# Optimization experiments

Measured on AMD Instinct MI355X. Metric: run time of the kernel, lower is better.

The kernel has to match this reference:

```python
import jax, jax.numpy as jnp
import numpy as np
from jax import lax

LR, SB, LB = 256, 16, 8  # lr_size, spatial_bin, luma_bins
DN = ('NCHW', 'OIHW', 'NCHW')


def conv2d(x, w, b=None, stride=1, pad=1):
    out = lax.conv_general_dilated(x, w, (stride, stride), [(pad, pad), (pad, pad)], dimension_numbers=DN)
    return out if b is None else out + b[None, :, None, None]


def gaussian_blur17(x):
    # kornia GaussianBlur2d(kernel=(17,17), sigma=(2,2)), reflect padding, separable
    t = jnp.arange(17, dtype=x.dtype) - 8.0
    g = jnp.exp(-(t * t) / 8.0)  # 2*sigma^2 = 8
    g = g / g.sum()
    C = x.shape[1]
    xp = jnp.pad(x, ((0, 0), (0, 0), (8, 8), (8, 8)), mode='reflect')
    kh = jnp.broadcast_to(g.reshape(1, 1, 17, 1), (C, 1, 17, 1))
    kw = jnp.broadcast_to(g.reshape(1, 1, 1, 17), (C, 1, 1, 17))
    x1 = lax.conv_general_dilated(xp, kh, (1, 1), 'VALID', dimension_numbers=DN, feature_group_count=C)
    return lax.conv_general_dilated(x1, kw, (1, 1), 'VALID', dimension_numbers=DN, feature_group_count=C)


def nearest_resize(x, size):
    # torch F.interpolate mode='nearest': src = floor(dst * in/out)
    H, W = x.shape[-2], x.shape[-1]
    iy = jnp.floor(jnp.arange(size) * (H / size)).astype(jnp.int32)
    ix = jnp.floor(jnp.arange(size) * (W / size)).astype(jnp.int32)
    return x[:, :, iy][:, :, :, ix]


def grid_sample_3d_border(inp, grid):
    # inp [B,C,D,Hi,Wi]; grid [B,Do,Ho,Wo,3] with (x,y,z); bilinear, padding_mode='border', align_corners=False
    B, C, D, Hi, Wi = inp.shape
    x = jnp.clip(((grid[..., 0] + 1.0) * Wi - 1.0) * 0.5, 0.0, Wi - 1.0)
    y = jnp.clip(((grid[..., 1] + 1.0) * Hi - 1.0) * 0.5, 0.0, Hi - 1.0)
    z = jnp.clip(((grid[..., 2] + 1.0) * D - 1.0) * 0.5, 0.0, D - 1.0)
    x0 = jnp.floor(x); y0 = jnp.floor(y); z0 = jnp.floor(z)
    fx = (x - x0)[:, None]; fy = (y - y0)[:, None]; fz = (z - z0)[:, None]  # [B,1,Do,Ho,Wo]
    x0i = x0.astype(jnp.int32); y0i = y0.astype(jnp.int32); z0i = z0.astype(jnp.int32)
    x1i = jnp.minimum(x0i + 1, Wi - 1); y1i = jnp.minimum(y0i + 1, Hi - 1); z1i = jnp.minimum(z0i + 1, D - 1)
    flat = inp.reshape(B, C, D * Hi * Wi)
    M = grid.shape[1] * grid.shape[2] * grid.shape[3]

    def gat(zi, yi, xi):
        idx = ((zi * Hi + yi) * Wi + xi).reshape(B, 1, M)
        v = jnp.take_along_axis(flat, jnp.broadcast_to(idx, (B, C, M)), axis=2)
        return v.reshape(B, C, grid.shape[1], grid.shape[2], grid.shape[3])

    return (gat(z0i, y0i, x0i) * (1 - fz) * (1 - fy) * (1 - fx)
            + gat(z0i, y0i, x1i) * (1 - fz) * (1 - fy) * fx
            + gat(z0i, y1i, x0i) * (1 - fz) * fy * (1 - fx)
            + gat(z0i, y1i, x1i) * (1 - fz) * fy * fx
            + gat(z1i, y0i, x0i) * fz * (1 - fy) * (1 - fx)
            + gat(z1i, y0i, x1i) * fz * (1 - fy) * fx
            + gat(z1i, y1i, x0i) * fz * fy * (1 - fx)
            + gat(z1i, y1i, x1i) * fz * fy * fx)


def _forward(lqs, evs, gw1, gb1, gw2, gb2, sw0, sb0, sw1, sb1, sw2, sb2, sw3, sb3,
             cw0, cb0, cw1, cb1, fw1, fb1, fw2, fb2, fw3, fb3, lw1, lb1, lw2, fuw, fub):
    B, _, H, W = lqs.shape
    # --- HighresStreamNet guide ---
    g = gaussian_blur17(lqs)
    g = jax.nn.relu(conv2d(g, gw1, gb1, 1, 0))
    guide = jax.nn.sigmoid(conv2d(g, gw2, gb2, 1, 0)) * 2.0 - 0.5  # [B,1,H,W]
    # --- slicing grid (x,y in (-0.5,1.5) per source, z = guide) ---
    gx = (jnp.arange(W, dtype=lqs.dtype) + 0.5) / W * 2.0 - 0.5
    gy = (jnp.arange(H, dtype=lqs.dtype) + 0.5) / H * 2.0 - 0.5
    gyy, gxx = jnp.meshgrid(gy, gx, indexing='ij')
    base = jnp.broadcast_to(jnp.stack([gxx, gyy], -1)[None, None], (B, 1, H, W, 2))
    grid = jnp.concatenate([base, guide[..., None]], axis=-1)  # [B,1,H,W,3]
    # --- LowresStreamNet ---
    lr = nearest_resize(lqs, LR)
    ev = evs if (evs.shape[-1] == LR and evs.shape[-2] == LR) else nearest_resize(evs, LR)
    x = jnp.concatenate([lr, ev], axis=1)  # [B,18,256,256]
    for w_, b_ in ((sw0, sb0), (sw1, sb1), (sw2, sb2), (sw3, sb3)):
        x = jax.nn.relu(conv2d(x, w_, b_, 2, 1))  # -> [B,64,16,16]
    xl = conv2d(jax.nn.relu(conv2d(x, lw1, lb1, 1, 1)), lw2, None, 1, 1)  # local, last conv no bias
    xg = jax.nn.relu(conv2d(x, cw0, cb0, 2, 1))
    xg = jax.nn.relu(conv2d(xg, cw1, cb1, 2, 1)).reshape(B, -1)  # [B,1024]
    xg = jax.nn.relu(xg @ fw1.T + fb1)
    xg = jax.nn.relu(xg @ fw2.T + fb2)
    xg = xg @ fw3.T + fb3  # [B,64]
    fused = jax.nn.relu(xg[:, :, None, None] + xl)
    bg = conv2d(fused, fuw, fub, 1, 0).reshape(B, 1, LB, SB, SB)  # bilateral grid [B,1,8,16,16]
    hr = grid_sample_3d_border(bg, grid)  # [B,1,1,H,W]
    return hr.reshape(B, -1, H, W)


def setup_inputs():
    key = jax.random.key(0)
    ks = iter(jax.random.split(key, 40))

    def W_(shape):
        fan_in = int(np.prod(shape[1:]))
        return jax.random.normal(next(ks), shape, jnp.float32) * np.float32(np.sqrt(2.0 / fan_in))

    def Z(n):
        return jnp.zeros((n,), jnp.float32)

    B, H, Wd = 8, 1024, 1024
    return {
        'lqs': jax.random.uniform(next(ks), (B, 3, H, Wd), jnp.float32),
        'evs': jax.random.normal(next(ks), (B, 15, 256, 256), jnp.float32) * 0.1,
        'gw1': W_((16, 3, 1, 1)), 'gb1': Z(16), 'gw2': W_((1, 16, 1, 1)), 'gb2': Z(1),
        'sw0': W_((8, 18, 3, 3)), 'sb0': Z(8), 'sw1': W_((16, 8, 3, 3)), 'sb1': Z(16),
        'sw2': W_((32, 16, 3, 3)), 'sb2': Z(32), 'sw3': W_((64, 32, 3, 3)), 'sb3': Z(64),
        'cw0': W_((64, 64, 3, 3)), 'cb0': Z(64), 'cw1': W_((64, 64, 3, 3)), 'cb1': Z(64),
        'fw1': W_((256, 1024)), 'fb1': Z(256), 'fw2': W_((128, 256)), 'fb2': Z(128),
        'fw3': W_((64, 128)), 'fb3': Z(64),
        'lw1': W_((64, 64, 3, 3)), 'lb1': Z(64), 'lw2': W_((64, 64, 3, 3)),
        'fuw': W_((8, 64, 1, 1)), 'fub': Z(8),
    }


def reference(lqs, evs, gw1, gb1, gw2, gb2, sw0, sb0, sw1, sb1, sw2, sb2, sw3, sb3,
              cw0, cb0, cw1, cb1, fw1, fb1, fw2, fb2, fw3, fb3, lw1, lb1, lw2, fuw, fub):
    return _forward(lqs, evs, gw1, gb1, gw2, gb2, sw0, sb0, sw1, sb1, sw2, sb2, sw3, sb3,
                    cw0, cb0, cw1, cb1, fw1, fb1, fw2, fb2, fw3, fb3, lw1, lb1, lw2, fuw, fub)
```

## Files before the change

### kernel.cpp

```cpp
#include <hip/hip_runtime.h>
#include <hip/hip_bf16.h>
#include <math.h>

#define BATCH 8
#define HH 1024
#define WW 1024

__device__ __forceinline__ int reflect1024(int i) {
    i = i < 0 ? -i : i;
    return i > 1023 ? 2046 - i : i;
}

__global__ __launch_bounds__(256) void conv0_k(const float* __restrict__ lqs,
                                               const float* __restrict__ evs,
                                               const float* __restrict__ w,
                                               const float* __restrict__ bias,
                                               float* __restrict__ out) {
    int idx = blockIdx.x * 256 + threadIdx.x;
    int q = idx & 4095;
    int b = idx >> 12;
    int qx = q & 31, oy = q >> 5;
    int iy0 = oy * 2 - 1;

    float acc[4][8];
#pragma unroll
    for (int j = 0; j < 4; ++j)
#pragma unroll
        for (int o = 0; o < 8; ++o) acc[j][o] = bias[o];

#pragma unroll
    for (int ic = 0; ic < 3; ++ic) {
        const float* ipc = lqs + (size_t)(b * 3 + ic) * HH * WW;
#pragma unroll
        for (int ky = 0; ky < 3; ++ky) {
            int iy = iy0 + ky;
            if (iy < 0) continue;
            const float* row = ipc + (size_t)iy * 4 * WW;
            float xr[9];
#pragma unroll
            for (int i = 0; i < 9; ++i) {
                int ix = 8 * qx - 1 + i;
                xr[i] = (ix >= 0) ? row[ix * 4] : 0.0f;
            }
#pragma unroll
            for (int o = 0; o < 8; ++o) {
                const float* wp = w + (o * 18 + ic) * 9 + ky * 3;
#pragma unroll
                for (int j = 0; j < 4; ++j)
#pragma unroll
                    for (int kx = 0; kx < 3; ++kx)
                        acc[j][o] = fmaf(wp[kx], xr[2 * j + kx], acc[j][o]);
            }
        }
    }
    for (int ic = 0; ic < 15; ++ic) {
        const float* ipc = evs + (size_t)(b * 15 + ic) * 65536;
#pragma unroll
        for (int ky = 0; ky < 3; ++ky) {
            int iy = iy0 + ky;
            if (iy < 0) continue;
            const float* row = ipc + iy * 256;
            const float4* r4 = (const float4*)row;
            float4 A = r4[2 * qx];
            float4 Bv = r4[2 * qx + 1];
            float m = (qx > 0) ? row[8 * qx - 1] : 0.0f;
            float xr[9] = {m, A.x, A.y, A.z, A.w, Bv.x, Bv.y, Bv.z, Bv.w};
#pragma unroll
            for (int o = 0; o < 8; ++o) {
                const float* wp = w + (o * 18 + ic + 3) * 9 + ky * 3;
#pragma unroll
                for (int j = 0; j < 4; ++j)
#pragma unroll
                    for (int kx = 0; kx < 3; ++kx)
                        acc[j][o] = fmaf(wp[kx], xr[2 * j + kx], acc[j][o]);
            }
        }
    }
#pragma unroll
    for (int o = 0; o < 8; ++o) {
        float4 v = make_float4(fmaxf(acc[0][o], 0.0f), fmaxf(acc[1][o], 0.0f),
                               fmaxf(acc[2][o], 0.0f), fmaxf(acc[3][o], 0.0f));
        *(float4*)(out + ((size_t)(b * 8 + o) << 14) + oy * 128 + qx * 4) = v;
    }
}

template <int IC, int OC, int OCT, int IH, int IW, int STRIDE, bool RELU, bool HASB>
__global__ __launch_bounds__(256) void convN_k(const float* __restrict__ in,
                                               const float* __restrict__ w,
                                               const float* __restrict__ bias,
                                               float* __restrict__ out) {
    constexpr int OH = (IH + 2 - 3) / STRIDE + 1;
    constexpr int OW = (IW + 2 - 3) / STRIDE + 1;
    constexpr int POS = OH * OW;
    constexpr int G = OC / OCT;
    int idx = blockIdx.x * 256 + threadIdx.x;
    if (idx >= BATCH * G * POS) return;
    int px = idx % POS;
    int g = (idx / POS) % G;
    int b = idx / (POS * G);
    int ox = px % OW, oy = px / OW;
    int iy0 = oy * STRIDE - 1, ix0 = ox * STRIDE - 1;

    float acc[OCT];
#pragma unroll
    for (int o = 0; o < OCT; ++o) acc[o] = HASB ? bias[g * OCT + o] : 0.0f;

    const float* ip = in + (size_t)b * IC * IH * IW;
    for (int ic = 0; ic < IC; ++ic) {
        const float* ipc = ip + ic * IH * IW;
        float x[9];
#pragma unroll
        for (int ky = 0; ky < 3; ++ky) {
            int iy = iy0 + ky;
#pragma unroll
            for (int kx = 0; kx < 3; ++kx) {
                int ix = ix0 + kx;
                bool ok = (iy >= 0) && (iy < IH) && (ix >= 0) && (ix < IW);
                x[ky * 3 + kx] = ok ? ipc[iy * IW + ix] : 0.0f;
            }
        }
#pragma unroll
        for (int o = 0; o < OCT; ++o) {
            const float* wp = w + ((g * OCT + o) * IC + ic) * 9;
#pragma unroll
            for (int k = 0; k < 9; ++k) acc[o] = fmaf(wp[k], x[k], acc[o]);
        }
    }
#pragma unroll
    for (int o = 0; o < OCT; ++o) {
        float v = acc[o];
        if (RELU) v = fmaxf(v, 0.0f);
        out[(size_t)(b * OC + g * OCT + o) * POS + px] = v;
    }
}

template <int IC, int OC, int OCT, int IH, int IW, int STRIDE, int SPLIT>
__global__ __launch_bounds__(256) void convS_k(const float* __restrict__ in,
                                               const float* __restrict__ w,
                                               float* __restrict__ part) {
    constexpr int OH = (IH + 2 - 3) / STRIDE + 1;
    constexpr int OW = (IW + 2 - 3) / STRIDE + 1;
    constexpr int POS = OH * OW;
    constexpr int G = OC / OCT;
    constexpr int TOT = BATCH * G * POS;
    constexpr int ICS = IC / SPLIT;
    constexpr int N = BATCH * OC * POS;
    int idx = blockIdx.x * 256 + threadIdx.x;
    if (idx >= TOT * SPLIT) return;
    int s = idx / TOT, r = idx % TOT;
    int px = r % POS;
    int g = (r / POS) % G;
    int b = r / (POS * G);
    int ox = px % OW, oy = px / OW;
    int iy0 = oy * STRIDE - 1, ix0 = ox * STRIDE - 1;

    float acc[OCT];
#pragma unroll
    for (int o = 0; o < OCT; ++o) acc[o] = 0.0f;

    const float* ip = in + (size_t)b * IC * IH * IW;
    for (int ic = s * ICS; ic < (s + 1) * ICS; ++ic) {
        const float* ipc = ip + ic * IH * IW;
        float x[9];
#pragma unroll
        for (int ky = 0; ky < 3; ++ky) {
            int iy = iy0 + ky;
#pragma unroll
            for (int kx = 0; kx < 3; ++kx) {
                int ix = ix0 + kx;
                bool ok = (iy >= 0) && (iy < IH) && (ix >= 0) && (ix < IW);
                x[ky * 3 + kx] = ok ? ipc[iy * IW + ix] : 0.0f;
            }
        }
#pragma unroll
        for (int o = 0; o < OCT; ++o) {
            const float* wp = w + ((g * OCT + o) * IC + ic) * 9;
#pragma unroll
            for (int k = 0; k < 9; ++k) acc[o] = fmaf(wp[k], x[k], acc[o]);
        }
    }
#pragma unroll
    for (int o = 0; o < OCT; ++o)
        part[(size_t)s * N + (size_t)(b * OC + g * OCT + o) * POS + px] = acc[o];
}

template <int OC, int POS, int SPLIT, bool RELU, bool HASB>
__global__ __launch_bounds__(256) void reduce_k(const float* __restrict__ part,
                                                const float* __restrict__ bias,
                                                float* __restrict__ out) {
    constexpr int N = BATCH * OC * POS;
    int idx = blockIdx.x * 256 + threadIdx.x;
    if (idx >= N) return;
    int oc = (idx / POS) % OC;
    float a = HASB ? bias[oc] : 0.0f;
#pragma unroll
    for (int s = 0; s < SPLIT; ++s) a += part[(size_t)s * N + idx];
    out[idx] = RELU ? fmaxf(a, 0.0f) : a;
}

__global__ __launch_bounds__(256) void fc1_k(const float* __restrict__ part_cw1,
                                             const float* __restrict__ cb1,
                                             const float* __restrict__ fw1,
                                             const float* __restrict__ fb1,
                                             float* __restrict__ h1) {
    __shared__ float xin[1024];
    int t = threadIdx.x;
    int b = blockIdx.x >> 6;
    int rgrp = blockIdx.x & 63;
    int wave = t >> 6, lane = t & 63;

    for (int i = t; i < 1024; i += 256) {
        float v = cb1[i >> 4];
#pragma unroll
        for (int s = 0; s < 16; ++s) v += part_cw1[s * 8192 + b * 1024 + i];
        xin[i] = fmaxf(v, 0.0f);
    }
    __syncthreads();

    int r = (rgrp << 2) | wave;
    const float4* w4 = (const float4*)(fw1 + r * 1024);
    const float4* x4 = (const float4*)xin;
    float acc = 0.0f;
#pragma unroll
    for (int jj = 0; jj < 4; ++jj) {
        float4 wv = w4[lane + 64 * jj];
        float4 xv = x4[lane + 64 * jj];
        acc = fmaf(wv.x, xv.x, acc);
        acc = fmaf(wv.y, xv.y, acc);
        acc = fmaf(wv.z, xv.z, acc);
        acc = fmaf(wv.w, xv.w, acc);
    }
#pragma unroll
    for (int m = 32; m; m >>= 1) acc += __shfl_xor(acc, m, 64);
    if (lane == 0) h1[b * 256 + r] = fmaxf(acc + fb1[r], 0.0f);
}

__global__ __launch_bounds__(256) void fc2_k(const float* __restrict__ h1,
                                             const float* __restrict__ fw2,
                                             const float* __restrict__ fb2,
                                             float* __restrict__ h2) {
    int t = threadIdx.x;
    int b = blockIdx.x >> 5;
    int rgrp = blockIdx.x & 31;
    int wave = t >> 6, lane = t & 63;
    int r = (rgrp << 2) | wave;
    float4 wv = ((const float4*)(fw2 + r * 256))[lane];
    float4 xv = ((const float4*)(h1 + b * 256))[lane];
    float acc = fmaf(wv.x, xv.x, fmaf(wv.y, xv.y, fmaf(wv.z, xv.z, wv.w * xv.w)));
#pragma unroll
    for (int m = 32; m; m >>= 1) acc += __shfl_xor(acc, m, 64);
    if (lane == 0) h2[b * 128 + r] = fmaxf(acc + fb2[r], 0.0f);
}

__global__ __launch_bounds__(256) void fc3_k(const float* __restrict__ h2,
                                             const float* __restrict__ fw3,
                                             const float* __restrict__ fb3,
                                             float* __restrict__ xgv) {
    int t = threadIdx.x;
    int b = blockIdx.x >> 4;
    int rgrp = blockIdx.x & 15;
    int wave = t >> 6, lane = t & 63;
    int r = (rgrp << 2) | wave;
    float2 wv = ((const float2*)(fw3 + r * 128))[lane];
    float2 xv = ((const float2*)(h2 + b * 128))[lane];
    float acc = fmaf(wv.x, xv.x, wv.y * xv.y);
#pragma unroll
    for (int m = 32; m; m >>= 1) acc += __shfl_xor(acc, m, 64);
    if (lane == 0) xgv[b * 64 + r] = acc + fb3[r];
}

__global__ __launch_bounds__(256) void fuse_k(const float* __restrict__ xg,
                                              const float* __restrict__ part_lw2,
                                              const float* __restrict__ fuw,
                                              const float* __restrict__ fub,
                                              float* __restrict__ bg) {
    int px = threadIdx.x;
    int d = blockIdx.x & 7;
    int b = blockIdx.x >> 3;
    float acc = fub[d];
    for (int c = 0; c < 64; ++c) {
        int base = (b * 64 + c) * 256 + px;
        float xlv = 0.0f;
#pragma unroll
        for (int s = 0; s < 8; ++s) xlv += part_lw2[s * 131072 + base];
        float f = fmaxf(xg[b * 64 + c] + xlv, 0.0f);
        acc = fmaf(fuw[d * 64 + c], f, acc);
    }
    bg[(b * 8 + d) * 256 + px] = acc;
}

__global__ __launch_bounds__(256) void guide_slice_k(const float* __restrict__ lqs,
                                                     const float* __restrict__ bgp,
                                                     const float* __restrict__ gw1,
                                                     const float* __restrict__ gb1,
                                                     const float* __restrict__ gw2,
                                                     const float* __restrict__ gb2,
                                                     float* __restrict__ out) {
    constexpr int TW = 64, TH = 32;
    __shared__ float sBH[3][TH][81];
    __shared__ float sBG[2048];
    __shared__ float sW1[48], sB1[16], sW2[16], sB2v[1];

    int t = threadIdx.x;
    int bx = blockIdx.x & 15;
    int by = (blockIdx.x >> 4) & 31;
    int b = blockIdx.x >> 9;
    int x0 = bx * TW, y0 = by * TH;

    float gv[17];
    {
        float gs = 0.0f;
#pragma unroll
        for (int i = 0; i < 17; ++i) {
            float d = (float)i - 8.0f;
            gv[i] = expf(-(d * d) * 0.125f);
            gs += gv[i];
        }
        float inv = 1.0f / gs;
#pragma unroll
        for (int i = 0; i < 17; ++i) gv[i] *= inv;
    }

    for (int i = t; i < 2048; i += 256) sBG[i] = bgp[b * 2048 + i];
    if (t < 48) sW1[t] = gw1[t];
    if (t < 16) { sB1[t] = gb1[t]; sW2[t] = gw2[t]; }
    if (t == 0) sB2v[0] = gb2[0];

    if (t < 240) {
        int c = t / 80, xo = t % 80;
        int gx = reflect1024(x0 + xo - 8);
        const float* colp = lqs + (size_t)(b * 3 + c) * HH * WW + gx;
        float win[17];
#pragma unroll
        for (int i = 0; i < 16; ++i)
            win[i] = colp[(size_t)reflect1024(y0 - 8 + i) * WW];
#pragma unroll
        for (int j = 0; j < TH; ++j) {
            win[(16 + j) % 17] = colp[(size_t)reflect1024(y0 + 8 + j) * WW];
            float acc = 0.0f;
#pragma unroll
            for (int i = 0; i < 17; ++i) acc = fmaf(gv[i], win[(j + i) % 17], acc);
            sBH[c][j][xo] = acc;
        }
    }
    __syncthreads();

    int yy = t >> 3, xs = (t & 7) * 8;
    int Y = y0 + yy;
    float fy = fminf(fmaxf((Y + 0.5f) * (1.0f / 64.0f) + 3.5f, 0.0f), 15.0f);
    float yf = floorf(fy);
    int yi = (int)yf;
    float ay = fy - yf;
    int yi1 = min(yi + 1, 15);

    float bcv[3][8];
#pragma unroll
    for (int c = 0; c < 3; ++c) {
        float win[17];
#pragma unroll
        for (int i = 0; i < 16; ++i) win[i] = sBH[c][yy][xs + i];
#pragma unroll
        for (int j = 0; j < 8; ++j) {
            win[(16 + j) % 17] = sBH[c][yy][xs + 16 + j];
            float acc = 0.0f;
#pragma unroll
            for (int i = 0; i < 17; ++i) acc = fmaf(gv[i], win[(j + i) % 17], acc);
            bcv[c][j] = acc;
        }
    }

    float val[8];
#pragma unroll
    for (int j = 0; j < 8; ++j) {
        float b0 = bcv[0][j], b1 = bcv[1][j], b2 = bcv[2][j];
        float s = sB2v[0];
#pragma unroll
        for (int c = 0; c < 16; ++c) {
            float g1 = fmaf(sW1[c * 3 + 0], b0,
                       fmaf(sW1[c * 3 + 1], b1,
                       fmaf(sW1[c * 3 + 2], b2, sB1[c])));
            s = fmaf(sW2[c], fmaxf(g1, 0.0f), s);
        }
        float sig = 1.0f / (1.0f + expf(-s));
        float guide = sig * 2.0f - 0.5f;

        int X = x0 + xs + j;
        float fx = fminf(fmaxf((X + 0.5f) * (1.0f / 64.0f) + 3.5f, 0.0f), 15.0f);
        float fz = fminf(fmaxf(fmaf(guide, 4.0f, 3.5f), 0.0f), 7.0f);
        float xf = floorf(fx), zf = floorf(fz);
        int xi = (int)xf, zi = (int)zf;
        float ax = fx - xf, az = fz - zf;
        int xi1 = min(xi + 1, 15), zi1 = min(zi + 1, 7);

        const float* g0 = sBG + zi * 256;
        const float* g1p = sBG + zi1 * 256;
        int i00 = yi * 16 + xi, i01 = yi * 16 + xi1;
        int i10 = yi1 * 16 + xi, i11 = yi1 * 16 + xi1;
        float c00 = g0[i00] + az * (g1p[i00] - g0[i00]);
        float c01 = g0[i01] + az * (g1p[i01] - g0[i01]);
        float c10 = g0[i10] + az * (g1p[i10] - g0[i10]);
        float c11 = g0[i11] + az * (g1p[i11] - g0[i11]);
        float c0 = c00 + ay * (c10 - c00);
        float c1 = c01 + ay * (c11 - c01);
        val[j] = c0 + ax * (c1 - c0);
    }
    float4* op = (float4*)(out + (size_t)b * HH * WW + (size_t)Y * WW + x0 + xs);
    op[0] = make_float4(val[0], val[1], val[2], val[3]);
    op[1] = make_float4(val[4], val[5], val[6], val[7]);
}

extern "C" void kernel_launch(void* const* d_in, const int* in_sizes, int n_in,
                              void* d_out, int out_size, void* d_ws, size_t ws_size,
                              hipStream_t stream) {
    const float* lqs = (const float*)d_in[0];
    const float* evs = (const float*)d_in[1];
    const float* gw1 = (const float*)d_in[2];
    const float* gb1 = (const float*)d_in[3];
    const float* gw2 = (const float*)d_in[4];
    const float* gb2 = (const float*)d_in[5];
    const float* sw0 = (const float*)d_in[6];
    const float* sb0 = (const float*)d_in[7];
    const float* sw1 = (const float*)d_in[8];
    const float* sb1 = (const float*)d_in[9];
    const float* sw2 = (const float*)d_in[10];
    const float* sb2 = (const float*)d_in[11];
    const float* sw3 = (const float*)d_in[12];
    const float* sb3 = (const float*)d_in[13];
    const float* cw0 = (const float*)d_in[14];
    const float* cb0 = (const float*)d_in[15];
    const float* cw1 = (const float*)d_in[16];
    const float* cb1 = (const float*)d_in[17];
    const float* fw1 = (const float*)d_in[18];
    const float* fb1 = (const float*)d_in[19];
    const float* fw2 = (const float*)d_in[20];
    const float* fb2 = (const float*)d_in[21];
    const float* fw3 = (const float*)d_in[22];
    const float* fb3 = (const float*)d_in[23];
    const float* lw1 = (const float*)d_in[24];
    const float* lb1 = (const float*)d_in[25];
    const float* lw2 = (const float*)d_in[26];
    const float* fuw = (const float*)d_in[27];
    const float* fub = (const float*)d_in[28];
    float* out = (float*)d_out;

    float* ws = (float*)d_ws;
    float* o0 = ws;
    float* o1 = o0 + 1048576;
    float* o2 = o1 + 524288;
    float* o3 = o2 + 262144;
    float* xl1 = o3 + 131072;
    float* xg0 = xl1 + 131072;
    float* xgv = xg0 + 32768;
    float* bg = xgv + 512;
    float* h1 = bg + 16384;
    float* h2 = h1 + 2048;
    float* partA = h2 + 1024;
    float* part_lw2 = partA + 1048576;
    float* part_cw1 = part_lw2 + 1048576;

    conv0_k<<<128, 256, 0, stream>>>(lqs, evs, sw0, sb0, o0);
    convN_k<8, 16, 8, 128, 128, 2, true, true><<<256, 256, 0, stream>>>(o0, sw1, sb1, o1);
    convS_k<16, 32, 8, 64, 64, 2, 4><<<512, 256, 0, stream>>>(o1, sw2, partA);
    reduce_k<32, 1024, 4, true, true><<<1024, 256, 0, stream>>>(partA, sb2, o2);
    convS_k<32, 64, 8, 32, 32, 2, 8><<<512, 256, 0, stream>>>(o2, sw3, partA);
    reduce_k<64, 256, 8, true, true><<<512, 256, 0, stream>>>(partA, sb3, o3);
    convS_k<64, 64, 8, 16, 16, 1, 8><<<512, 256, 0, stream>>>(o3, lw1, partA);
    reduce_k<64, 256, 8, true, true><<<512, 256, 0, stream>>>(partA, lb1, xl1);
    convS_k<64, 64, 8, 16, 16, 1, 8><<<512, 256, 0, stream>>>(xl1, lw2, part_lw2);
    convS_k<64, 64, 8, 16, 16, 2, 16><<<256, 256, 0, stream>>>(o3, cw0, partA);
    reduce_k<64, 64, 16, true, true><<<128, 256, 0, stream>>>(partA, cb0, xg0);
    convS_k<64, 64, 4, 8, 8, 2, 16><<<128, 256, 0, stream>>>(xg0, cw1, part_cw1);
    fc1_k<<<512, 256, 0, stream>>>(part_cw1, cb1, fw1, fb1, h1);
    fc2_k<<<256, 256, 0, stream>>>(h1, fw2, fb2, h2);
    fc3_k<<<128, 256, 0, stream>>>(h2, fw3, fb3, xgv);
    fuse_k<<<64, 256, 0, stream>>>(xgv, part_lw2, fuw, fub, bg);
    guide_slice_k<<<BATCH * 32 * 16, 256, 0, stream>>>(lqs, bg, gw1, gb1, gw2, gb2, out);
}
```

Baseline: 400.2 us.

## Replace split-K conv+reduce passes with direct convs and fuse fc2/fc3/fuse

Mid-network convolutions previously used split-K partial sums plus separate reduce kernels. They now use the direct convN_k kernel with bias and ReLU applied in place. The fc2, fc3 and fuse stages are merged into one per-batch kernel that keeps intermediates in shared memory. This cuts launches and partial-sum traffic, but each direct conv thread now does more serial work, and the fused tail runs on only 8 blocks.

```diff
diff --git a/kernel.cpp b/kernel.cpp
--- a/kernel.cpp
+++ b/kernel.cpp
@@ -184,20 +184,6 @@
         part[(size_t)s * N + (size_t)(b * OC + g * OCT + o) * POS + px] = acc[o];
 }
 
-template <int OC, int POS, int SPLIT, bool RELU, bool HASB>
-__global__ __launch_bounds__(256) void reduce_k(const float* __restrict__ part,
-                                                const float* __restrict__ bias,
-                                                float* __restrict__ out) {
-    constexpr int N = BATCH * OC * POS;
-    int idx = blockIdx.x * 256 + threadIdx.x;
-    if (idx >= N) return;
-    int oc = (idx / POS) % OC;
-    float a = HASB ? bias[oc] : 0.0f;
-#pragma unroll
-    for (int s = 0; s < SPLIT; ++s) a += part[(size_t)s * N + idx];
-    out[idx] = RELU ? fmaxf(a, 0.0f) : a;
-}
-
 __global__ __launch_bounds__(256) void fc1_k(const float* __restrict__ part_cw1,
                                              const float* __restrict__ cb1,
                                              const float* __restrict__ fw1,
@@ -235,58 +221,55 @@
     if (lane == 0) h1[b * 256 + r] = fmaxf(acc + fb1[r], 0.0f);
 }
 
-__global__ __launch_bounds__(256) void fc2_k(const float* __restrict__ h1,
-                                             const float* __restrict__ fw2,
-                                             const float* __restrict__ fb2,
-                                             float* __restrict__ h2) {
-    int t = threadIdx.x;
-    int b = blockIdx.x >> 5;
-    int rgrp = blockIdx.x & 31;
+__global__ __launch_bounds__(256) void fc23fuse_k(const float* __restrict__ h1,
+                                                  const float* __restrict__ fw2,
+                                                  const float* __restrict__ fb2,
+                                                  const float* __restrict__ fw3,
+                                                  const float* __restrict__ fb3,
+                                                  const float* __restrict__ xl2,
+                                                  const float* __restrict__ fuw,
+                                                  const float* __restrict__ fub,
+                                                  float* __restrict__ bg) {
+    __shared__ float h2[128];
+    __shared__ float xg[64];
+    int b = blockIdx.x, t = threadIdx.x;
     int wave = t >> 6, lane = t & 63;
-    int r = (rgrp << 2) | wave;
-    float4 wv = ((const float4*)(fw2 + r * 256))[lane];
-    float4 xv = ((const float4*)(h1 + b * 256))[lane];
-    float acc = fmaf(wv.x, xv.x, fmaf(wv.y, xv.y, fmaf(wv.z, xv.z, wv.w * xv.w)));
-#pragma unroll
-    for (int m = 32; m; m >>= 1) acc += __shfl_xor(acc, m, 64);
-    if (lane == 0) h2[b * 128 + r] = fmaxf(acc + fb2[r], 0.0f);
-}
-
-__global__ __launch_bounds__(256) void fc3_k(const float* __restrict__ h2,
-                                             const float* __restrict__ fw3,
-                                             const float* __restrict__ fb3,
-                                             float* __restrict__ xgv) {
-    int t = threadIdx.x;
-    int b = blockIdx.x >> 4;
-    int rgrp = blockIdx.x & 15;
-    int wave = t >> 6, lane = t & 63;
-    int r = (rgrp << 2) | wave;
-    float2 wv = ((const float2*)(fw3 + r * 128))[lane];
-    float2 xv = ((const float2*)(h2 + b * 128))[lane];
-    float acc = fmaf(wv.x, xv.x, wv.y * xv.y);
-#pragma unroll
-    for (int m = 32; m; m >>= 1) acc += __shfl_xor(acc, m, 64);
-    if (lane == 0) xgv[b * 64 + r] = acc + fb3[r];
-}
-
-__global__ __launch_bounds__(256) void fuse_k(const float* __restrict__ xg,
-                                              const float* __restrict__ part_lw2,
-                                              const float* __restrict__ fuw,
-                                              const float* __restrict__ fub,
-                                              float* __restrict__ bg) {
-    int px = threadIdx.x;
-    int d = blockIdx.x & 7;
-    int b = blockIdx.x >> 3;
-    float acc = fub[d];
+
+    float4 xv1 = ((const float4*)(h1 + b * 256))[lane];
+#pragma unroll 4
+    for (int i = 0; i < 32; ++i) {
+        int r = wave * 32 + i;
+        float4 wv = ((const float4*)(fw2 + r * 256))[lane];
+        float acc = fmaf(wv.x, xv1.x, fmaf(wv.y, xv1.y, fmaf(wv.z, xv1.z, wv.w * xv1.w)));
+#pragma unroll
+        for (int m = 32; m; m >>= 1) acc += __shfl_xor(acc, m, 64);
+        if (lane == 0) h2[r] = fmaxf(acc + fb2[r], 0.0f);
+    }
+    __syncthreads();
+
+    float2 xv2 = ((const float2*)h2)[lane];
+#pragma unroll 4
+    for (int i = 0; i < 16; ++i) {
+        int r = wave * 16 + i;
+        float2 wv = ((const float2*)(fw3 + r * 128))[lane];
+        float acc = fmaf(wv.x, xv2.x, wv.y * xv2.y);
+#pragma unroll
+        for (int m = 32; m; m >>= 1) acc += __shfl_xor(acc, m, 64);
+        if (lane == 0) xg[r] = acc + fb3[r];
+    }
+    __syncthreads();
+
+    int px = t;
+    float acc[8];
+#pragma unroll
+    for (int d = 0; d < 8; ++d) acc[d] = fub[d];
     for (int c = 0; c < 64; ++c) {
-        int base = (b * 64 + c) * 256 + px;
-        float xlv = 0.0f;
-#pragma unroll
-        for (int s = 0; s < 8; ++s) xlv += part_lw2[s * 131072 + base];
-        float f = fmaxf(xg[b * 64 + c] + xlv, 0.0f);
-        acc = fmaf(fuw[d * 64 + c], f, acc);
-    }
-    bg[(b * 8 + d) * 256 + px] = acc;
+        float f = fmaxf(xg[c] + xl2[(b * 64 + c) * 256 + px], 0.0f);
+#pragma unroll
+        for (int d = 0; d < 8; ++d) acc[d] = fmaf(fuw[d * 64 + c], f, acc[d]);
+    }
+#pragma unroll
+    for (int d = 0; d < 8; ++d) bg[(b * 8 + d) * 256 + px] = acc[d];
 }
 
 __global__ __launch_bounds__(256) void guide_slice_k(const float* __restrict__ lqs,
@@ -449,30 +432,21 @@
     float* o2 = o1 + 524288;
     float* o3 = o2 + 262144;
     float* xl1 = o3 + 131072;
-    float* xg0 = xl1 + 131072;
-    float* xgv = xg0 + 32768;
-    float* bg = xgv + 512;
-    float* h1 = bg + 16384;
-    float* h2 = h1 + 2048;
-    float* partA = h2 + 1024;
-    float* part_lw2 = partA + 1048576;
-    float* part_cw1 = part_lw2 + 1048576;
+    float* xl2 = xl1 + 131072;
+    float* xg0 = xl2 + 131072;
+    float* h1 = xg0 + 32768;
+    float* bg = h1 + 2048;
+    float* part_cw1 = bg + 16384;
 
     conv0_k<<<128, 256, 0, stream>>>(lqs, evs, sw0, sb0, o0);
-    convN_k<8, 16, 8, 128, 128, 2, true, true><<<256, 256, 0, stream>>>(o0, sw1, sb1, o1);
-    convS_k<16, 32, 8, 64, 64, 2, 4><<<512, 256, 0, stream>>>(o1, sw2, partA);
-    reduce_k<32, 1024, 4, true, true><<<1024, 256, 0, stream>>>(partA, sb2, o2);
-    convS_k<32, 64, 8, 32, 32, 2, 8><<<512, 256, 0, stream>>>(o2, sw3, partA);
-    reduce_k<64, 256, 8, true, true><<<512, 256, 0, stream>>>(partA, sb3, o3);
-    convS_k<64, 64, 8, 16, 16, 1, 8><<<512, 256, 0, stream>>>(o3, lw1, partA);
-    reduce_k<64, 256, 8, true, true><<<512, 256, 0, stream>>>(partA, lb1, xl1);
-    convS_k<64, 64, 8, 16, 16, 1, 8><<<512, 256, 0, stream>>>(xl1, lw2, part_lw2);
-    convS_k<64, 64, 8, 16, 16, 2, 16><<<256, 256, 0, stream>>>(o3, cw0, partA);
-    reduce_k<64, 64, 16, true, true><<<128, 256, 0, stream>>>(partA, cb0, xg0);
+    convN_k<8, 16, 4, 128, 128, 2, true, true><<<512, 256, 0, stream>>>(o0, sw1, sb1, o1);
+    convN_k<16, 32, 2, 64, 64, 2, true, true><<<512, 256, 0, stream>>>(o1, sw2, sb2, o2);
+    convN_k<32, 64, 1, 32, 32, 2, true, true><<<512, 256, 0, stream>>>(o2, sw3, sb3, o3);
+    convN_k<64, 64, 1, 16, 16, 1, true, true><<<512, 256, 0, stream>>>(o3, lw1, lb1, xl1);
+    convN_k<64, 64, 1, 16, 16, 1, false, false><<<512, 256, 0, stream>>>(xl1, lw2, nullptr, xl2);
+    convN_k<64, 64, 1, 16, 16, 2, true, true><<<128, 256, 0, stream>>>(o3, cw0, cb0, xg0);
     convS_k<64, 64, 4, 8, 8, 2, 16><<<128, 256, 0, stream>>>(xg0, cw1, part_cw1);
     fc1_k<<<512, 256, 0, stream>>>(part_cw1, cb1, fw1, fb1, h1);
-    fc2_k<<<256, 256, 0, stream>>>(h1, fw2, fb2, h2);
-    fc3_k<<<128, 256, 0, stream>>>(h2, fw3, fb3, xgv);
-    fuse_k<<<64, 256, 0, stream>>>(xgv, part_lw2, fuw, fub, bg);
+    fc23fuse_k<<<8, 256, 0, stream>>>(h1, fw2, fb2, fw3, fb3, xl2, fuw, fub, bg);
     guide_slice_k<<<BATCH * 32 * 16, 256, 0, stream>>>(lqs, bg, gw1, gb1, gw2, gb2, out);
 }
```

Result: slower. 485.1 us (+21.2%).
